# Performance work log

Measured on AMD Instinct MI355X. Metric: run time of the kernel, lower is better.

The kernel has to match this reference:

```python
import jax, jax.numpy as jnp
import numpy as np

N_GAUSS = 2048
FEAT_DIM = 3
IMG_H, IMG_W = 256, 256
EPS = 1e-4  # args.eps with tiled rasterizer path


def setup_inputs() -> dict:
    key = jax.random.key(0)
    k_xy, k_sc, k_rot, k_feat = jax.random.split(key, 4)
    xy = jax.random.uniform(k_xy, (N_GAUSS, 2), dtype=jnp.float32)  # normalized [0,1) coords
    # scale holds INVERSE std-devs (disable_inverse_scale=False path: scale = 1/init_scale);
    # values 10..50 give Gaussians spanning a few pixels at 256x256.
    scale = jax.random.uniform(k_sc, (N_GAUSS, 2), minval=10.0, maxval=50.0, dtype=jnp.float32)
    rot = jax.random.normal(k_rot, (N_GAUSS, 1), dtype=jnp.float32)
    feat = jax.random.uniform(k_feat, (N_GAUSS, FEAT_DIM), dtype=jnp.float32)
    return {"xy": xy, "scale": scale, "rot": rot, "feat": feat, "topk": 8}


def reference(xy, scale, rot, feat, topk):
    # Pixel centers in normalized coordinates, matching get_grid(h, w) -> (x, y)
    xs = (jnp.arange(IMG_W, dtype=jnp.float32) + 0.5) / IMG_W
    ys = (jnp.arange(IMG_H, dtype=jnp.float32) + 0.5) / IMG_H
    px, py = jnp.meshgrid(xs, ys, indexing="xy")  # each [H, W]
    px = px.reshape(-1)  # [P]
    py = py.reshape(-1)

    dx = px[:, None] - xy[None, :, 0]  # [P, N]
    dy = py[:, None] - xy[None, :, 1]  # [P, N]

    c = jnp.cos(rot[:, 0])  # [N]
    s = jnp.sin(rot[:, 0])
    # Rotate offset into the Gaussian's local frame
    lx = dx * c + dy * s   # [P, N]
    ly = -dx * s + dy * c  # [P, N]

    # Anisotropic Gaussian weight; scale is the inverse std-dev per axis
    w = jnp.exp(-0.5 * ((lx * scale[:, 0]) ** 2 + (ly * scale[:, 1]) ** 2))  # [P, N]

    # Keep top-k Gaussians per pixel, normalize their weights, accumulate features
    tw, ti = jax.lax.top_k(w, topk)        # [P, K]
    tf = feat[ti]                          # [P, K, C]
    alpha = tw / (jnp.sum(tw, axis=-1, keepdims=True) + EPS)  # [P, K]
    img = jnp.einsum("pk,pkc->pc", alpha, tf)                 # [P, C]
    return img.reshape(IMG_H, IMG_W, FEAT_DIM).transpose(2, 0, 1)  # [C, H, W]
```

## Files before the change

### kernel.cpp

```cpp
#include <hip/hip_runtime.h>
#include <math.h>

#define N_GAUSS 2048
#define IMG_H 256
#define IMG_W 256
#define NPIX (IMG_H * IMG_W)
#define EPS 1e-4f

#define TILE 8
#define TILES_X (IMG_W / TILE)
#define NTILES (TILES_X * (IMG_H / TILE))
#define SEG 512
#define SEGCAP 128
#define D_HALF 0.019336f

#define LADDER(T, G)                                                     \
    if ((T) < v7) {                                                      \
        const bool c0 = (T) < v0, c1 = (T) < v1, c2 = (T) < v2;          \
        const bool c3 = (T) < v3, c4 = (T) < v4, c5 = (T) < v5;          \
        const bool c6 = (T) < v6;                                        \
        v7 = c6 ? v6 : (T);            i7 = c6 ? i6 : (G);               \
        v6 = c6 ? (c5 ? v5 : (T)) : v6; i6 = c6 ? (c5 ? i5 : (G)) : i6;  \
        v5 = c5 ? (c4 ? v4 : (T)) : v5; i5 = c5 ? (c4 ? i4 : (G)) : i5;  \
        v4 = c4 ? (c3 ? v3 : (T)) : v4; i4 = c4 ? (c3 ? i3 : (G)) : i4;  \
        v3 = c3 ? (c2 ? v2 : (T)) : v3; i3 = c3 ? (c2 ? i2 : (G)) : i3;  \
        v2 = c2 ? (c1 ? v1 : (T)) : v2; i2 = c2 ? (c1 ? i1 : (G)) : i2;  \
        v1 = c1 ? (c0 ? v0 : (T)) : v1; i1 = c1 ? (c0 ? i0 : (G)) : i1;  \
        v0 = c0 ? (T) : v0;            i0 = c0 ? (G) : i0;               \
    }

#define CE(a, i, j)                                   \
    { float lo_ = fminf(a[i], a[j]);                  \
      float hi_ = fmaxf(a[i], a[j]);                  \
      a[i] = lo_; a[j] = hi_; }

#define SORT8(a)                                      \
    CE(a,0,1) CE(a,2,3) CE(a,4,5) CE(a,6,7)           \
    CE(a,0,2) CE(a,1,3) CE(a,4,6) CE(a,5,7)           \
    CE(a,1,2) CE(a,5,6)                               \
    CE(a,0,4) CE(a,1,5) CE(a,2,6) CE(a,3,7)           \
    CE(a,2,4) CE(a,3,5)                               \
    CE(a,1,2) CE(a,3,4) CE(a,5,6)

#define MERGE8(A, B)                                  \
    { float t_[8];                                    \
      t_[0] = fminf(A[0], B[7]); t_[1] = fminf(A[1], B[6]); \
      t_[2] = fminf(A[2], B[5]); t_[3] = fminf(A[3], B[4]); \
      t_[4] = fminf(A[4], B[3]); t_[5] = fminf(A[5], B[2]); \
      t_[6] = fminf(A[6], B[1]); t_[7] = fminf(A[7], B[0]); \
      CE(t_,0,4) CE(t_,1,5) CE(t_,2,6) CE(t_,3,7)     \
      CE(t_,0,2) CE(t_,1,3) CE(t_,4,6) CE(t_,5,7)     \
      CE(t_,0,1) CE(t_,2,3) CE(t_,4,5) CE(t_,6,7)     \
      A[0]=t_[0]; A[1]=t_[1]; A[2]=t_[2]; A[3]=t_[3]; \
      A[4]=t_[4]; A[5]=t_[5]; A[6]=t_[6]; A[7]=t_[7]; }

__device__ __forceinline__ void top8_butterfly(float (&cur)[8]) {
#pragma unroll
    for (int m = 1; m < 64; m <<= 1) {
        float oth[8];
#pragma unroll
        for (int k = 0; k < 8; ++k) oth[k] = __shfl_xor(cur[k], m, 64);
        float t_[8];
#pragma unroll
        for (int k = 0; k < 8; ++k) t_[k] = fminf(cur[k], oth[7 - k]);
        CE(t_,0,4) CE(t_,1,5) CE(t_,2,6) CE(t_,3,7)
        CE(t_,0,2) CE(t_,1,3) CE(t_,4,6) CE(t_,5,7)
        CE(t_,0,1) CE(t_,2,3) CE(t_,4,5) CE(t_,6,7)
#pragma unroll
        for (int k = 0; k < 8; ++k) cur[k] = t_[k];
    }
}

__global__ void prep_kernel(const float* __restrict__ xy,
                            const float* __restrict__ scale,
                            const float* __restrict__ rot,
                            float4* __restrict__ gA,
                            float4* __restrict__ gB,
                            float4* __restrict__ gC) {
    int g = blockIdx.x * blockDim.x + threadIdx.x;
    if (g >= N_GAUSS) return;
    float x  = xy[2 * g + 0];
    float y  = xy[2 * g + 1];
    float sx = scale[2 * g + 0];
    float sy = scale[2 * g + 1];
    double r = (double)rot[g];
    float c = (float)cos(r);
    float s = (float)sin(r);
    gA[g] = make_float4(x, y, c * sx, s * sx);
    gB[g] = make_float4(-s * sy, c * sy, fmaxf(sx, sy) * D_HALF, 0.f);
    gC[g] = make_float4(c, s, sx, sy);
}

__launch_bounds__(256)
__global__ void fused_kernel(const float* __restrict__ xy,
                             const float4* __restrict__ gA,
                             const float4* __restrict__ gB,
                             const float4* __restrict__ gC,
                             const float* __restrict__ feat,
                             float* __restrict__ out) {
    __shared__ float rlo[N_GAUSS];
    __shared__ float wlist[4][8];
    __shared__ float s_cut;
    __shared__ unsigned short qidx[N_GAUSS];
    __shared__ int qcnt[4];
    __shared__ float4 cps[4 * SEGCAP];
    __shared__ float2 csc[4 * SEGCAP];
    __shared__ float          lt[4][8][64];
    __shared__ unsigned short li[4][8][64];

    const int tid  = threadIdx.x;
    const int lane = tid & 63;
    const int w    = tid >> 6;
    const int tile = blockIdx.x;

    const float cx = (float)((tile & (TILES_X - 1)) * TILE + 4) * (1.0f / IMG_W);
    const float cy = (float)((tile / TILES_X) * TILE + 4) * (1.0f / IMG_H);
    float cur[8];
#pragma unroll
    for (int r = 0; r < N_GAUSS / 256; ++r) {
        int g = r * 256 + tid;
        float4 a = gA[g];
        float4 b = gB[g];
        float dx = cx - a.x;
        float dy = cy - a.y;
        float lx = dx * a.z + dy * a.w;
        float ly = dx * b.x + dy * b.y;
        float rr = sqrtf(lx * lx + ly * ly);
        rlo[g]  = rr - b.z;
        cur[r]  = rr + b.z;
    }
    SORT8(cur)

    top8_butterfly(cur);
    if (lane == 0) {
#pragma unroll
        for (int k = 0; k < 8; ++k) wlist[w][k] = cur[k];
    }
    __syncthreads();

    if (tid == 0) {
        float A[8], B[8], C2[8], D2[8];
#pragma unroll
        for (int k = 0; k < 8; ++k) {
            A[k]  = wlist[0][k];
            B[k]  = wlist[1][k];
            C2[k] = wlist[2][k];
            D2[k] = wlist[3][k];
        }
        MERGE8(A, B)
        MERGE8(C2, D2)
        MERGE8(A, C2)
        float cut = A[7];
        s_cut = cut + 0.01f + 1e-4f * cut;
    }
    __syncthreads();
    const float cut = s_cut;

    {
        const int segbase = w * SEG;
        unsigned base = 0;
        for (int s2 = 0; s2 < SEG / 64; ++s2) {
            int g = segbase + s2 * 64 + lane;
            bool keep = rlo[g] <= cut;
            unsigned long long mask = __ballot(keep);
            if (keep) {
                unsigned pos = base + (unsigned)__popcll(mask & ((1ull << lane) - 1ull));
                qidx[segbase + pos] = (unsigned short)g;
                if (pos < SEGCAP) {
                    float4 a = gA[g];
                    float4 e = gC[g];
                    cps[w * SEGCAP + pos] = make_float4(a.x, a.y, e.x, e.y);
                    csc[w * SEGCAP + pos] = make_float2(e.z, e.w);
                }
            }
            base += (unsigned)__popcll(mask);
        }
        if (lane == 0) qcnt[w] = (int)base;
    }
    __syncthreads();

    const int pxi = (tile & (TILES_X - 1)) * TILE + (lane & 7);
    const int pyi = (tile / TILES_X) * TILE + (lane >> 3);
    const int p   = pyi * IMG_W + pxi;
    const float px = (pxi + 0.5f) * (1.0f / IMG_W);
    const float py = (pyi + 0.5f) * (1.0f / IMG_H);

    float v0 = INFINITY, v1 = INFINITY, v2 = INFINITY, v3 = INFINITY;
    float v4 = INFINITY, v5 = INFINITY, v6 = INFINITY, v7 = INFINITY;
    int   i0 = 0, i1 = 0, i2 = 0, i3 = 0, i4 = 0, i5 = 0, i6 = 0, i7 = 0;

#define PROC_EXACT(AX, AY, AC, AS, BX, BY, G)                            \
    {                                                                    \
        float dx = __fsub_rn(px, (AX));                                  \
        float dy = __fsub_rn(py, (AY));                                  \
        float lx = __fadd_rn(__fmul_rn(dx, (AC)), __fmul_rn(dy, (AS)));  \
        float ly = __fadd_rn(__fmul_rn(-dx, (AS)), __fmul_rn(dy, (AC))); \
        float aa = __fmul_rn(lx, (BX));                                  \
        float bb = __fmul_rn(ly, (BY));                                  \
        float t2 = __fadd_rn(__fmul_rn(aa, aa), __fmul_rn(bb, bb));      \
        LADDER(t2, (G))                                                  \
    }

    {
        const int segbase = w * SEG;
        const int cnt  = qcnt[w];
        const int jcap = cnt < SEGCAP ? cnt : SEGCAP;
        for (int j = 0; j < jcap; ++j) {
            float4 a4 = cps[w * SEGCAP + j];
            float2 b2 = csc[w * SEGCAP + j];
            int    g  = (int)qidx[segbase + j];
            PROC_EXACT(a4.x, a4.y, a4.z, a4.w, b2.x, b2.y, g)
        }
        for (int j = SEGCAP; j < cnt; ++j) {
            int    g  = (int)qidx[segbase + j];
            float4 a  = gA[g];
            float4 e  = gC[g];
            PROC_EXACT(a.x, a.y, e.x, e.y, e.z, e.w, g)
        }
    }
#undef PROC_EXACT

    lt[w][0][lane] = v0; li[w][0][lane] = (unsigned short)i0;
    lt[w][1][lane] = v1; li[w][1][lane] = (unsigned short)i1;
    lt[w][2][lane] = v2; li[w][2][lane] = (unsigned short)i2;
    lt[w][3][lane] = v3; li[w][3][lane] = (unsigned short)i3;
    lt[w][4][lane] = v4; li[w][4][lane] = (unsigned short)i4;
    lt[w][5][lane] = v5; li[w][5][lane] = (unsigned short)i5;
    lt[w][6][lane] = v6; li[w][6][lane] = (unsigned short)i6;
    lt[w][7][lane] = v7; li[w][7][lane] = (unsigned short)i7;
    __syncthreads();

    if (w == 0) {
        v0 = INFINITY; v1 = INFINITY; v2 = INFINITY; v3 = INFINITY;
        v4 = INFINITY; v5 = INFINITY; v6 = INFINITY; v7 = INFINITY;
        i0 = 0; i1 = 0; i2 = 0; i3 = 0; i4 = 0; i5 = 0; i6 = 0; i7 = 0;
        for (int c = 0; c < 4; ++c) {
#pragma unroll
            for (int k = 0; k < 8; ++k) {
                float t2 = lt[c][k][lane];
                int   g  = (int)li[c][k][lane];
                LADDER(t2, g)
            }
        }
        float w0 = expf(-0.5f * v0), w1 = expf(-0.5f * v1);
        float w2 = expf(-0.5f * v2), w3 = expf(-0.5f * v3);
        float w4 = expf(-0.5f * v4), w5 = expf(-0.5f * v5);
        float w6 = expf(-0.5f * v6), w7 = expf(-0.5f * v7);
        float sum = w0 + w1 + w2 + w3 + w4 + w5 + w6 + w7;
        float inv = 1.0f / (sum + EPS);

        float oc0 = 0.f, oc1 = 0.f, oc2 = 0.f;
#define ACC(K)                                                  \
        {                                                       \
            float al = w##K * inv;                              \
            const float* f = feat + 3 * i##K;                   \
            oc0 = fmaf(al, f[0], oc0);                          \
            oc1 = fmaf(al, f[1], oc1);                          \
            oc2 = fmaf(al, f[2], oc2);                          \
        }
        ACC(0) ACC(1) ACC(2) ACC(3) ACC(4) ACC(5) ACC(6) ACC(7)
#undef ACC

        out[p]            = oc0;
        out[p + NPIX]     = oc1;
        out[p + 2 * NPIX] = oc2;
    }
}

extern "C" void kernel_launch(void* const* d_in, const int* in_sizes, int n_in,
                              void* d_out, int out_size, void* d_ws, size_t ws_size,
                              hipStream_t stream) {
    const float* xy    = (const float*)d_in[0];
    const float* scale = (const float*)d_in[1];
    const float* rot   = (const float*)d_in[2];
    const float* feat  = (const float*)d_in[3];
    float* out = (float*)d_out;

    float4* gA = (float4*)d_ws;
    float4* gB = gA + N_GAUSS;
    float4* gC = gB + N_GAUSS;

    prep_kernel<<<N_GAUSS / 256, 256, 0, stream>>>(xy, scale, rot, gA, gB, gC);
    fused_kernel<<<NTILES, 256, 0, stream>>>(xy, gA, gB, gC, feat, out);
}
```

Before: 27.45 us.

## Fuse Gaussian preprocessing into rasterizer and use per-wave culling cutoffs

Drops the separate prep kernel. Each wave now loads raw xy, scale and rot for its own 512-Gaussian segment into registers and computes the culling bounds with fast __sincosf. The cutoff is taken from each wave's own butterfly top-8 rather than a block-wide merge, which removes the shared-memory merge and two block barriers. Exact double-precision sincos is computed only for the surviving candidates, staged in LDS. This saves a kernel launch and a global round trip, in exchange for redundant bound work in every tile block and a looser per-wave cutoff that may keep more candidates.

```diff
diff --git a/kernel.cpp b/kernel.cpp
--- a/kernel.cpp
+++ b/kernel.cpp
@@ -42,18 +42,6 @@
     CE(a,2,4) CE(a,3,5)                               \
     CE(a,1,2) CE(a,3,4) CE(a,5,6)
 
-#define MERGE8(A, B)                                  \
-    { float t_[8];                                    \
-      t_[0] = fminf(A[0], B[7]); t_[1] = fminf(A[1], B[6]); \
-      t_[2] = fminf(A[2], B[5]); t_[3] = fminf(A[3], B[4]); \
-      t_[4] = fminf(A[4], B[3]); t_[5] = fminf(A[5], B[2]); \
-      t_[6] = fminf(A[6], B[1]); t_[7] = fminf(A[7], B[0]); \
-      CE(t_,0,4) CE(t_,1,5) CE(t_,2,6) CE(t_,3,7)     \
-      CE(t_,0,2) CE(t_,1,3) CE(t_,4,6) CE(t_,5,7)     \
-      CE(t_,0,1) CE(t_,2,3) CE(t_,4,5) CE(t_,6,7)     \
-      A[0]=t_[0]; A[1]=t_[1]; A[2]=t_[2]; A[3]=t_[3]; \
-      A[4]=t_[4]; A[5]=t_[5]; A[6]=t_[6]; A[7]=t_[7]; }
-
 __device__ __forceinline__ void top8_butterfly(float (&cur)[8]) {
 #pragma unroll
     for (int m = 1; m < 64; m <<= 1) {
@@ -70,124 +58,6 @@
         for (int k = 0; k < 8; ++k) cur[k] = t_[k];
     }
 }
-
-__global__ void prep_kernel(const float* __restrict__ xy,
-                            const float* __restrict__ scale,
-                            const float* __restrict__ rot,
-                            float4* __restrict__ gA,
-                            float4* __restrict__ gB,
-                            float4* __restrict__ gC) {
-    int g = blockIdx.x * blockDim.x + threadIdx.x;
-    if (g >= N_GAUSS) return;
-    float x  = xy[2 * g + 0];
-    float y  = xy[2 * g + 1];
-    float sx = scale[2 * g + 0];
-    float sy = scale[2 * g + 1];
-    double r = (double)rot[g];
-    float c = (float)cos(r);
-    float s = (float)sin(r);
-    gA[g] = make_float4(x, y, c * sx, s * sx);
-    gB[g] = make_float4(-s * sy, c * sy, fmaxf(sx, sy) * D_HALF, 0.f);
-    gC[g] = make_float4(c, s, sx, sy);
-}
-
-__launch_bounds__(256)
-__global__ void fused_kernel(const float* __restrict__ xy,
-                             const float4* __restrict__ gA,
-                             const float4* __restrict__ gB,
-                             const float4* __restrict__ gC,
-                             const float* __restrict__ feat,
-                             float* __restrict__ out) {
-    __shared__ float rlo[N_GAUSS];
-    __shared__ float wlist[4][8];
-    __shared__ float s_cut;
-    __shared__ unsigned short qidx[N_GAUSS];
-    __shared__ int qcnt[4];
-    __shared__ float4 cps[4 * SEGCAP];
-    __shared__ float2 csc[4 * SEGCAP];
-    __shared__ float          lt[4][8][64];
-    __shared__ unsigned short li[4][8][64];
-
-    const int tid  = threadIdx.x;
-    const int lane = tid & 63;
-    const int w    = tid >> 6;
-    const int tile = blockIdx.x;
-
-    const float cx = (float)((tile & (TILES_X - 1)) * TILE + 4) * (1.0f / IMG_W);
-    const float cy = (float)((tile / TILES_X) * TILE + 4) * (1.0f / IMG_H);
-    float cur[8];
-#pragma unroll
-    for (int r = 0; r < N_GAUSS / 256; ++r) {
-        int g = r * 256 + tid;
-        float4 a = gA[g];
-        float4 b = gB[g];
-        float dx = cx - a.x;
-        float dy = cy - a.y;
-        float lx = dx * a.z + dy * a.w;
-        float ly = dx * b.x + dy * b.y;
-        float rr = sqrtf(lx * lx + ly * ly);
-        rlo[g]  = rr - b.z;
-        cur[r]  = rr + b.z;
-    }
-    SORT8(cur)
-
-    top8_butterfly(cur);
-    if (lane == 0) {
-#pragma unroll
-        for (int k = 0; k < 8; ++k) wlist[w][k] = cur[k];
-    }
-    __syncthreads();
-
-    if (tid == 0) {
-        float A[8], B[8], C2[8], D2[8];
-#pragma unroll
-        for (int k = 0; k < 8; ++k) {
-            A[k]  = wlist[0][k];
-            B[k]  = wlist[1][k];
-            C2[k] = wlist[2][k];
-            D2[k] = wlist[3][k];
-        }
-        MERGE8(A, B)
-        MERGE8(C2, D2)
-        MERGE8(A, C2)
-        float cut = A[7];
-        s_cut = cut + 0.01f + 1e-4f * cut;
-    }
-    __syncthreads();
-    const float cut = s_cut;
-
-    {
-        const int segbase = w * SEG;
-        unsigned base = 0;
-        for (int s2 = 0; s2 < SEG / 64; ++s2) {
-            int g = segbase + s2 * 64 + lane;
-            bool keep = rlo[g] <= cut;
-            unsigned long long mask = __ballot(keep);
-            if (keep) {
-                unsigned pos = base + (unsigned)__popcll(mask & ((1ull << lane) - 1ull));
-                qidx[segbase + pos] = (unsigned short)g;
-                if (pos < SEGCAP) {
-                    float4 a = gA[g];
-                    float4 e = gC[g];
-                    cps[w * SEGCAP + pos] = make_float4(a.x, a.y, e.x, e.y);
-                    csc[w * SEGCAP + pos] = make_float2(e.z, e.w);
-                }
-            }
-            base += (unsigned)__popcll(mask);
-        }
-        if (lane == 0) qcnt[w] = (int)base;
-    }
-    __syncthreads();
-
-    const int pxi = (tile & (TILES_X - 1)) * TILE + (lane & 7);
-    const int pyi = (tile / TILES_X) * TILE + (lane >> 3);
-    const int p   = pyi * IMG_W + pxi;
-    const float px = (pxi + 0.5f) * (1.0f / IMG_W);
-    const float py = (pyi + 0.5f) * (1.0f / IMG_H);
-
-    float v0 = INFINITY, v1 = INFINITY, v2 = INFINITY, v3 = INFINITY;
-    float v4 = INFINITY, v5 = INFINITY, v6 = INFINITY, v7 = INFINITY;
-    int   i0 = 0, i1 = 0, i2 = 0, i3 = 0, i4 = 0, i5 = 0, i6 = 0, i7 = 0;
 
 #define PROC_EXACT(AX, AY, AC, AS, BX, BY, G)                            \
     {                                                                    \
@@ -201,24 +71,106 @@
         LADDER(t2, (G))                                                  \
     }
 
-    {
-        const int segbase = w * SEG;
-        const int cnt  = qcnt[w];
-        const int jcap = cnt < SEGCAP ? cnt : SEGCAP;
-        for (int j = 0; j < jcap; ++j) {
-            float4 a4 = cps[w * SEGCAP + j];
-            float2 b2 = csc[w * SEGCAP + j];
-            int    g  = (int)qidx[segbase + j];
-            PROC_EXACT(a4.x, a4.y, a4.z, a4.w, b2.x, b2.y, g)
-        }
-        for (int j = SEGCAP; j < cnt; ++j) {
-            int    g  = (int)qidx[segbase + j];
-            float4 a  = gA[g];
-            float4 e  = gC[g];
-            PROC_EXACT(a.x, a.y, e.x, e.y, e.z, e.w, g)
-        }
-    }
-#undef PROC_EXACT
+__launch_bounds__(256, 4)
+__global__ void fused_kernel(const float* __restrict__ xy,
+                             const float* __restrict__ scale,
+                             const float* __restrict__ rot,
+                             const float* __restrict__ feat,
+                             float* __restrict__ out) {
+    __shared__ float4 qa[4][SEGCAP];
+    __shared__ float  qr[4][SEGCAP];
+    __shared__ float2 qt[4][SEGCAP];
+    __shared__ unsigned short qidx[4][SEG];
+    __shared__ float          lt[4][8][64];
+    __shared__ unsigned short li[4][8][64];
+
+    const int tid  = threadIdx.x;
+    const int lane = tid & 63;
+    const int w    = tid >> 6;
+    const int tile = blockIdx.x;
+
+    const float cx = (float)((tile & (TILES_X - 1)) * TILE + 4) * (1.0f / IMG_W);
+    const float cy = (float)((tile / TILES_X) * TILE + 4) * (1.0f / IMG_H);
+
+    float2 xy_r[8], sc_r[8];
+    float  rot_r[8], rlo_r[8];
+    float  cur[8];
+#pragma unroll
+    for (int s = 0; s < 8; ++s) {
+        int g = w * SEG + s * 64 + lane;
+        xy_r[s]  = ((const float2*)xy)[g];
+        sc_r[s]  = ((const float2*)scale)[g];
+        rot_r[s] = rot[g];
+        float sn, cs2;
+        __sincosf(rot_r[s], &sn, &cs2);
+        float dx = cx - xy_r[s].x;
+        float dy = cy - xy_r[s].y;
+        float lx = dx * cs2 + dy * sn;
+        float ly = dy * cs2 - dx * sn;
+        float a  = lx * sc_r[s].x;
+        float b  = ly * sc_r[s].y;
+        float rr = sqrtf(a * a + b * b);
+        float m  = fmaxf(sc_r[s].x, sc_r[s].y) * D_HALF;
+        rlo_r[s] = rr - m;
+        cur[s]   = rr + m;
+    }
+
+    SORT8(cur)
+    top8_butterfly(cur);
+    float cut = cur[7];
+    cut = cut + 0.01f + 1e-4f * cut;
+
+    unsigned base = 0;
+#pragma unroll
+    for (int s = 0; s < 8; ++s) {
+        bool keep = rlo_r[s] <= cut;
+        unsigned long long mask = __ballot(keep);
+        if (keep) {
+            unsigned pos = base + (unsigned)__popcll(mask & ((1ull << lane) - 1ull));
+            qidx[w][pos] = (unsigned short)(w * SEG + s * 64 + lane);
+            if (pos < SEGCAP) {
+                qa[w][pos] = make_float4(xy_r[s].x, xy_r[s].y, sc_r[s].x, sc_r[s].y);
+                qr[w][pos] = rot_r[s];
+            }
+        }
+        base += (unsigned)__popcll(mask);
+    }
+    const int cnt = (int)base;
+
+    const int pxi = (tile & (TILES_X - 1)) * TILE + (lane & 7);
+    const int pyi = (tile / TILES_X) * TILE + (lane >> 3);
+    const int p   = pyi * IMG_W + pxi;
+    const float px = (pxi + 0.5f) * (1.0f / IMG_W);
+    const float py = (pyi + 0.5f) * (1.0f / IMG_H);
+
+    float v0 = INFINITY, v1 = INFINITY, v2 = INFINITY, v3 = INFINITY;
+    float v4 = INFINITY, v5 = INFINITY, v6 = INFINITY, v7 = INFINITY;
+    int   i0 = 0, i1 = 0, i2 = 0, i3 = 0, i4 = 0, i5 = 0, i6 = 0, i7 = 0;
+
+    const int jcap = cnt < SEGCAP ? cnt : SEGCAP;
+    for (int b = 0; b < jcap; b += 64) {
+        int t = b + lane;
+        if (t < jcap) {
+            double sd, cd;
+            sincos((double)qr[w][t], &sd, &cd);
+            qt[w][t] = make_float2((float)cd, (float)sd);
+        }
+        int lim = (b + 64 < jcap) ? b + 64 : jcap;
+        for (int j = b; j < lim; ++j) {
+            float4 a4 = qa[w][j];
+            float2 ct = qt[w][j];
+            int    g  = (int)qidx[w][j];
+            PROC_EXACT(a4.x, a4.y, ct.x, ct.y, a4.z, a4.w, g)
+        }
+    }
+    for (int j = SEGCAP; j < cnt; ++j) {
+        int g = (int)qidx[w][j];
+        float2 xyg = ((const float2*)xy)[g];
+        float2 scg = ((const float2*)scale)[g];
+        double sd, cd;
+        sincos((double)rot[g], &sd, &cd);
+        PROC_EXACT(xyg.x, xyg.y, (float)cd, (float)sd, scg.x, scg.y, g)
+    }
 
     lt[w][0][lane] = v0; li[w][0][lane] = (unsigned short)i0;
     lt[w][1][lane] = v1; li[w][1][lane] = (unsigned short)i1;
@@ -276,10 +228,5 @@
     const float* feat  = (const float*)d_in[3];
     float* out = (float*)d_out;
 
-    float4* gA = (float4*)d_ws;
-    float4* gB = gA + N_GAUSS;
-    float4* gC = gB + N_GAUSS;
-
-    prep_kernel<<<N_GAUSS / 256, 256, 0, stream>>>(xy, scale, rot, gA, gB, gC);
-    fused_kernel<<<NTILES, 256, 0, stream>>>(xy, gA, gB, gC, feat, out);
+    fused_kernel<<<NTILES, 256, 0, stream>>>(xy, scale, rot, feat, out);
 }
```

Measured after the change: 26.16 us. 1.05x faster.
